# Kernel optimization log

Hardware: AMD Instinct MI355X
Metric: run time of the kernel (lower is better)

The kernel has to match this reference:

```python
import jax, jax.numpy as jnp
import numpy as np

B, S, T = 32, 512, 20      # sentences, tokens/sentence, chars/word
N_CHARS = 128              # embedding rows = N_CHARS + 1 (0 is pad)
D = 128                    # char_dim
H = 256                    # char_lstm_dim


def _gru_last_state(x_tnd, mask_tn, Wk, Wr, b):
    """Keras GRU (reset_after=True, gate order z,r,h) over time-major input.
    x_tnd: [T, N, D], mask_tn: [T, N] bool. Masked steps pass state through.
    Returns final hidden state [N, H]."""
    h_dim = Wr.shape[0]
    b_in, b_rec = b[0], b[1]

    def step(h, inp):
        x, m = inp
        xg = x @ Wk + b_in            # [N, 3H]
        hg = h @ Wr + b_rec           # [N, 3H]
        xz, xr, xh = jnp.split(xg, 3, axis=-1)
        hz, hr, hh = jnp.split(hg, 3, axis=-1)
        z = jax.nn.sigmoid(xz + hz)
        r = jax.nn.sigmoid(xr + hr)
        hc = jnp.tanh(xh + r * hh)
        hn = z * h + (1.0 - z) * hc
        hn = jnp.where(m[:, None], hn, h)
        return hn, None

    h0 = jnp.zeros((x_tnd.shape[1], h_dim), dtype=x_tnd.dtype)
    hT, _ = jax.lax.scan(step, h0, (x_tnd, mask_tn))
    return hT


def setup_inputs() -> dict:
    key = jax.random.key(0)
    ks = jax.random.split(key, 8)
    inputs = jax.random.randint(ks[0], (B, S, T), 0, N_CHARS + 1, dtype=jnp.int32)
    sc = 0.05
    emb = jax.random.normal(ks[1], (N_CHARS + 1, D), dtype=jnp.float32) * sc
    Wk_f = jax.random.normal(ks[2], (D, 3 * H), dtype=jnp.float32) * sc
    Wr_f = jax.random.normal(ks[3], (H, 3 * H), dtype=jnp.float32) * sc
    b_f = jnp.zeros((2, 3 * H), dtype=jnp.float32)
    Wk_b = jax.random.normal(ks[4], (D, 3 * H), dtype=jnp.float32) * sc
    Wr_b = jax.random.normal(ks[5], (H, 3 * H), dtype=jnp.float32) * sc
    b_b = jnp.zeros((2, 3 * H), dtype=jnp.float32)
    return {"inputs": inputs, "emb": emb, "Wk_f": Wk_f, "Wr_f": Wr_f,
            "b_f": b_f, "Wk_b": Wk_b, "Wr_b": Wr_b, "b_b": b_b}


def reference(inputs, emb, Wk_f, Wr_f, b_f, Wk_b, Wr_b, b_b):
    bsz, seq, wlen = inputs.shape
    h_dim = Wr_f.shape[0]
    flat = inputs.reshape(bsz * seq, wlen)           # [N, T]
    mask = flat != 0                                 # [N, T] (0 = pad)
    x = emb[flat]                                    # [N, T, D]
    x_t = jnp.transpose(x, (1, 0, 2))                # [T, N, D]
    m_t = mask.T                                     # [T, N]
    h_fwd = _gru_last_state(x_t, m_t, Wk_f, Wr_f, b_f)
    # Bidirectional: backward layer sees the reversed sequence + reversed mask
    h_bwd = _gru_last_state(x_t[::-1], m_t[::-1], Wk_b, Wr_b, b_b)
    out = jnp.concatenate([h_fwd, h_bwd], axis=-1)   # [N, 2H]
    return out.reshape(bsz, seq, 2 * h_dim)
```

## Files before the change

kernel.cpp:

```cpp
#include <hip/hip_runtime.h>
#include <hip/hip_bf16.h>

#define TS 20
#define DNUM 128
#define HH 256
#define NWORDS 16384
#define WPB 16
#define GRPS 8
#define NBLK 256

typedef __attribute__((ext_vector_type(8))) short s8v;
typedef __attribute__((ext_vector_type(4))) float f4v;

#define L2E 1.4426950408889634f

__device__ __forceinline__ unsigned short bf16_rne(float f) {
  union { float f; unsigned u; } x; x.f = f;
  unsigned r = x.u + 0x7fffu + ((x.u >> 16) & 1u);
  return (unsigned short)(r >> 16);
}

__global__ void build_tab4(const float* __restrict__ emb,
                           const float* __restrict__ wkF, const float* __restrict__ bF,
                           const float* __restrict__ wkB, const float* __restrict__ bB,
                           float* __restrict__ tab4) {
  int gid = blockIdx.x * 256 + threadIdx.x;
  if (gid >= 2 * 129 * 768) return;
  int dir = gid / (129 * 768);
  int rem = gid - dir * (129 * 768);
  int c = rem / 768, j = rem - (rem / 768) * 768;
  int g = j >> 8, u = j & 255;
  const float* Wk = dir ? wkB : wkF;
  const float* bb = dir ? bB : bF;
  float s = bb[j];
  const float* er = emb + c * DNUM;
  #pragma unroll 4
  for (int d = 0; d < DNUM; ++d) s = fmaf(er[d], Wk[d * 768 + j], s);
  s *= (g == 2) ? (2.f * L2E) : (-L2E);
  tab4[((((size_t)dir * 129) + c) * 256 + u) * 4 + g] = s;
}

__global__ void pack_wr(const float* __restrict__ wrF, const float* __restrict__ wrB,
                        uint4* __restrict__ wp) {
  int gid = blockIdx.x * 256 + threadIdx.x;
  if (gid >= 2 * 48 * 8 * 64) return;
  int dir = gid / (48 * 8 * 64);
  int rem = gid - dir * (48 * 8 * 64);
  int ct = rem / (8 * 64);
  int kk = (rem / 64) & 7;
  int lane = rem & 63;
  const float* Wr = dir ? wrB : wrF;
  int n = ct * 16 + (lane & 15);
  int k0 = kk * 32 + (lane >> 4) * 8;
  const float sc = (ct >> 4) == 2 ? (2.f * L2E) : (-L2E);
  union { unsigned short v[8]; uint4 q; } u;
  #pragma unroll
  for (int e = 0; e < 8; ++e) u.v[e] = bf16_rne(sc * Wr[(k0 + e) * 768 + n]);
  wp[gid] = u.q;
}

__global__ __launch_bounds__(1024, 4) void gru_main(
    const int* __restrict__ chars, const float* __restrict__ tab4,
    const uint4* __restrict__ wrp, const float* __restrict__ bf_,
    const float* __restrict__ bb_, float* __restrict__ out) {
  const int bid = blockIdx.x;
  const int dir = bid >> 7;
  const int wslot = bid & 127;
  const float4* table = (const float4*)tab4 + (size_t)dir * 129 * 256;
  const uint4* WP = wrp + dir * (48 * 8 * 64);
  const float* brec = (dir ? bb_ : bf_) + 768;

  const int tid = threadIdx.x;
  const int w = tid >> 6, lane = tid & 63;
  const int lr = lane >> 4, lc = lane & 15;
  const int u = w * 16 + lc;

  __shared__ unsigned short hbf[2][WPB][HH + 8];
  __shared__ int sch[WPB * TS];
  __shared__ uint4 bhl[16 * 8 * 64];

  for (int i = tid; i < 16 * 8 * 64; i += 1024) bhl[i] = WP[16384 + i];

  uint4 Bz[8], Brr[8];
  #pragma unroll
  for (int kk = 0; kk < 8; ++kk) {
    Bz[kk]  = WP[((0 * 16 + w) * 8 + kk) * 64 + lane];
    Brr[kk] = WP[((1 * 16 + w) * 8 + kk) * 64 + lane];
  }

  const float br0 = -L2E * brec[0 * 256 + u];
  const float br1 = -L2E * brec[1 * 256 + u];
  const float br2 = 2.f * L2E * brec[2 * 256 + u];

  #pragma unroll 1
  for (int grp = 0; grp < GRPS; ++grp) {
    const int word0 = wslot * 128 + grp * WPB;

    for (int i = tid; i < WPB * (HH + 8) / 2; i += 1024)
      ((unsigned*)&hbf[0][0][0])[i] = 0;
    for (int i = tid; i < WPB * TS; i += 1024) sch[i] = chars[word0 * TS + i];

    float h[4];
    #pragma unroll
    for (int r = 0; r < 4; ++r) h[r] = 0.f;

    __syncthreads();

    #pragma unroll 1
    for (int t = 0; t < TS; ++t) {
      const int ts = dir ? (TS - 1 - t) : t;
      const int cur = t & 1;

      int cc[4];
      float4 xg[4];
      #pragma unroll
      for (int r = 0; r < 4; ++r) cc[r] = sch[(lr * 4 + r) * TS + ts];
      #pragma unroll
      for (int r = 0; r < 4; ++r) xg[r] = table[cc[r] * 256 + u];

      f4v a0 = {br0, br0, br0, br0};
      f4v a1 = {br1, br1, br1, br1};
      f4v a2 = {br2, br2, br2, br2};

      #pragma unroll
      for (int kk = 0; kk < 8; ++kk) {
        const uint4 av = *(const uint4*)&hbf[cur][lc][kk * 32 + lr * 8];
        const uint4 bh = bhl[(w * 8 + kk) * 64 + lane];
        const s8v aa = __builtin_bit_cast(s8v, av);
        a0 = __builtin_amdgcn_mfma_f32_16x16x32_bf16(aa, __builtin_bit_cast(s8v, Bz[kk]),  a0, 0, 0, 0);
        a1 = __builtin_amdgcn_mfma_f32_16x16x32_bf16(aa, __builtin_bit_cast(s8v, Brr[kk]), a1, 0, 0, 0);
        a2 = __builtin_amdgcn_mfma_f32_16x16x32_bf16(aa, __builtin_bit_cast(s8v, bh),      a2, 0, 0, 0);
      }

      #pragma unroll
      for (int r = 0; r < 4; ++r) {
        const int lw = lr * 4 + r;
        const float z  = __builtin_amdgcn_rcpf(1.f + __builtin_amdgcn_exp2f(xg[r].x + a0[r]));
        const float rr = __builtin_amdgcn_rcpf(1.f + __builtin_amdgcn_exp2f(xg[r].y + a1[r]));
        const float hc = fmaf(-2.f, __builtin_amdgcn_rcpf(
            1.f + __builtin_amdgcn_exp2f(fmaf(rr, a2[r], xg[r].z))), 1.f);
        const float hp = h[r];
        float hn = fmaf(1.f - z, hc - hp, hp);
        hn = (cc[r] != 0) ? hn : hp;
        h[r] = hn;
        hbf[cur ^ 1][lw][u] = bf16_rne(hn);
      }
      __syncthreads();
    }

    #pragma unroll
    for (int r = 0; r < 4; ++r) {
      const int lw = lr * 4 + r;
      out[(size_t)(word0 + lw) * 512 + dir * 256 + u] = h[r];
    }
    __syncthreads();
  }
}

extern "C" void kernel_launch(void* const* d_in, const int* in_sizes, int n_in,
                              void* d_out, int out_size, void* d_ws, size_t ws_size,
                              hipStream_t stream) {
  const int* chars = (const int*)d_in[0];
  const float* emb = (const float*)d_in[1];
  const float* wkF = (const float*)d_in[2];
  const float* wrF = (const float*)d_in[3];
  const float* bF  = (const float*)d_in[4];
  const float* wkB = (const float*)d_in[5];
  const float* wrB = (const float*)d_in[6];
  const float* bB  = (const float*)d_in[7];
  float* outp = (float*)d_out;

  float* tab4 = (float*)d_ws;
  uint4* wrp = (uint4*)((char*)d_ws + 2 * 129 * 256 * 16);

  build_tab4<<<(2 * 129 * 768 + 255) / 256, 256, 0, stream>>>(emb, wkF, bF, wkB, bB, tab4);
  pack_wr<<<(2 * 48 * 8 * 64 + 255) / 256, 256, 0, stream>>>(wrF, wrB, wrp);
  gru_main<<<NBLK, 1024, 0, stream>>>(chars, tab4, wrp, bF, bB, outp);
}
```

Measured before the change: 328.6 us.

## Process 32 words per group with single h buffer and split gate tables

Each block now runs 32 words per group (two 16-row MFMA tiles) in 4 groups instead of 16 words in 8 groups. This halves the number of sequential recurrence steps per block and reuses the register-held Wz/Wr fragments and LDS Wh fragments across two tiles. The double-buffered hidden state becomes a single buffer guarded by an extra barrier between the MFMA reads and the writes. The input-gate table is split into a z/r float2 table with the recurrent z/r bias folded in and a separate h table, and the lookups move after the MFMAs. The cost is more accumulator registers and one extra __syncthreads per timestep.

```diff
diff --git a/kernel.cpp b/kernel.cpp
--- a/kernel.cpp
+++ b/kernel.cpp
@@ -3,10 +3,7 @@
 
 #define TS 20
 #define DNUM 128
-#define HH 256
 #define NWORDS 16384
-#define WPB 16
-#define GRPS 8
 #define NBLK 256
 
 typedef __attribute__((ext_vector_type(8))) short s8v;
@@ -20,10 +17,10 @@
   return (unsigned short)(r >> 16);
 }
 
-__global__ void build_tab4(const float* __restrict__ emb,
-                           const float* __restrict__ wkF, const float* __restrict__ bF,
-                           const float* __restrict__ wkB, const float* __restrict__ bB,
-                           float* __restrict__ tab4) {
+__global__ void build_tab(const float* __restrict__ emb,
+                          const float* __restrict__ wkF, const float* __restrict__ bF,
+                          const float* __restrict__ wkB, const float* __restrict__ bB,
+                          float* __restrict__ tab2, float* __restrict__ tabh) {
   int gid = blockIdx.x * 256 + threadIdx.x;
   if (gid >= 2 * 129 * 768) return;
   int dir = gid / (129 * 768);
@@ -36,8 +33,8 @@
   const float* er = emb + c * DNUM;
   #pragma unroll 4
   for (int d = 0; d < DNUM; ++d) s = fmaf(er[d], Wk[d * 768 + j], s);
-  s *= (g == 2) ? (2.f * L2E) : (-L2E);
-  tab4[((((size_t)dir * 129) + c) * 256 + u) * 4 + g] = s;
+  if (g < 2) tab2[(((size_t)dir * 129 + c) * 256 + u) * 2 + g] = -L2E * (s + bb[768 + j]);
+  else       tabh[((size_t)dir * 129 + c) * 256 + u] = 2.f * L2E * s;
 }
 
 __global__ void pack_wr(const float* __restrict__ wrF, const float* __restrict__ wrB,
@@ -60,13 +57,15 @@
 }
 
 __global__ __launch_bounds__(1024, 4) void gru_main(
-    const int* __restrict__ chars, const float* __restrict__ tab4,
-    const uint4* __restrict__ wrp, const float* __restrict__ bf_,
-    const float* __restrict__ bb_, float* __restrict__ out) {
+    const int* __restrict__ chars, const float* __restrict__ tab2,
+    const float* __restrict__ tabh, const uint4* __restrict__ wrp,
+    const float* __restrict__ bf_, const float* __restrict__ bb_,
+    float* __restrict__ out) {
   const int bid = blockIdx.x;
   const int dir = bid >> 7;
   const int wslot = bid & 127;
-  const float4* table = (const float4*)tab4 + (size_t)dir * 129 * 256;
+  const float2* T2 = (const float2*)tab2 + (size_t)dir * 129 * 256;
+  const float*  TH = tabh + (size_t)dir * 129 * 256;
   const uint4* WP = wrp + dir * (48 * 8 * 64);
   const float* brec = (dir ? bb_ : bf_) + 768;
 
@@ -75,83 +74,99 @@
   const int lr = lane >> 4, lc = lane & 15;
   const int u = w * 16 + lc;
 
-  __shared__ unsigned short hbf[2][WPB][HH + 8];
-  __shared__ int sch[WPB * TS];
-  __shared__ uint4 bhl[16 * 8 * 64];
+  __shared__ uint4 bhl[8192];
+  __shared__ unsigned short hbf[32][272];
+  __shared__ int sch[32 * TS];
 
-  for (int i = tid; i < 16 * 8 * 64; i += 1024) bhl[i] = WP[16384 + i];
+  for (int i = tid; i < 8192; i += 1024) bhl[i] = WP[16384 + i];
 
-  uint4 Bz[8], Brr[8];
+  uint4 Wz[8], Wrr[8];
   #pragma unroll
   for (int kk = 0; kk < 8; ++kk) {
-    Bz[kk]  = WP[((0 * 16 + w) * 8 + kk) * 64 + lane];
-    Brr[kk] = WP[((1 * 16 + w) * 8 + kk) * 64 + lane];
+    Wz[kk]  = WP[((0 * 16 + w) * 8 + kk) * 64 + lane];
+    Wrr[kk] = WP[((16 + w) * 8 + kk) * 64 + lane];
   }
 
-  const float br0 = -L2E * brec[0 * 256 + u];
-  const float br1 = -L2E * brec[1 * 256 + u];
-  const float br2 = 2.f * L2E * brec[2 * 256 + u];
+  const float brh = 2.f * L2E * brec[512 + u];
 
   #pragma unroll 1
-  for (int grp = 0; grp < GRPS; ++grp) {
-    const int word0 = wslot * 128 + grp * WPB;
+  for (int grp = 0; grp < 4; ++grp) {
+    const int word0 = wslot * 128 + grp * 32;
 
-    for (int i = tid; i < WPB * (HH + 8) / 2; i += 1024)
-      ((unsigned*)&hbf[0][0][0])[i] = 0;
-    for (int i = tid; i < WPB * TS; i += 1024) sch[i] = chars[word0 * TS + i];
+    for (int i = tid; i < 32 * 272 / 2; i += 1024) ((unsigned*)&hbf[0][0])[i] = 0;
+    for (int i = tid; i < 32 * TS; i += 1024) sch[i] = chars[word0 * TS + i];
 
-    float h[4];
+    float h0[4], h1[4];
     #pragma unroll
-    for (int r = 0; r < 4; ++r) h[r] = 0.f;
+    for (int r = 0; r < 4; ++r) { h0[r] = 0.f; h1[r] = 0.f; }
 
     __syncthreads();
 
     #pragma unroll 1
     for (int t = 0; t < TS; ++t) {
       const int ts = dir ? (TS - 1 - t) : t;
-      const int cur = t & 1;
 
-      int cc[4];
-      float4 xg[4];
+      int cc0[4], cc1[4];
       #pragma unroll
-      for (int r = 0; r < 4; ++r) cc[r] = sch[(lr * 4 + r) * TS + ts];
-      #pragma unroll
-      for (int r = 0; r < 4; ++r) xg[r] = table[cc[r] * 256 + u];
+      for (int r = 0; r < 4; ++r) {
+        cc0[r] = sch[(lr * 4 + r) * TS + ts];
+        cc1[r] = sch[(16 + lr * 4 + r) * TS + ts];
+      }
 
-      f4v a0 = {br0, br0, br0, br0};
-      f4v a1 = {br1, br1, br1, br1};
-      f4v a2 = {br2, br2, br2, br2};
+      f4v a0z = {0.f, 0.f, 0.f, 0.f}, a0r = a0z, a0h = {brh, brh, brh, brh};
+      f4v a1z = a0z, a1r = a0z, a1h = a0h;
 
       #pragma unroll
       for (int kk = 0; kk < 8; ++kk) {
-        const uint4 av = *(const uint4*)&hbf[cur][lc][kk * 32 + lr * 8];
         const uint4 bh = bhl[(w * 8 + kk) * 64 + lane];
-        const s8v aa = __builtin_bit_cast(s8v, av);
-        a0 = __builtin_amdgcn_mfma_f32_16x16x32_bf16(aa, __builtin_bit_cast(s8v, Bz[kk]),  a0, 0, 0, 0);
-        a1 = __builtin_amdgcn_mfma_f32_16x16x32_bf16(aa, __builtin_bit_cast(s8v, Brr[kk]), a1, 0, 0, 0);
-        a2 = __builtin_amdgcn_mfma_f32_16x16x32_bf16(aa, __builtin_bit_cast(s8v, bh),      a2, 0, 0, 0);
+        const s8v aa0 = __builtin_bit_cast(s8v, *(const uint4*)&hbf[lc][kk * 32 + lr * 8]);
+        const s8v aa1 = __builtin_bit_cast(s8v, *(const uint4*)&hbf[16 + lc][kk * 32 + lr * 8]);
+        a0z = __builtin_amdgcn_mfma_f32_16x16x32_bf16(aa0, __builtin_bit_cast(s8v, Wz[kk]),  a0z, 0, 0, 0);
+        a0r = __builtin_amdgcn_mfma_f32_16x16x32_bf16(aa0, __builtin_bit_cast(s8v, Wrr[kk]), a0r, 0, 0, 0);
+        a0h = __builtin_amdgcn_mfma_f32_16x16x32_bf16(aa0, __builtin_bit_cast(s8v, bh),      a0h, 0, 0, 0);
+        a1z = __builtin_amdgcn_mfma_f32_16x16x32_bf16(aa1, __builtin_bit_cast(s8v, Wz[kk]),  a1z, 0, 0, 0);
+        a1r = __builtin_amdgcn_mfma_f32_16x16x32_bf16(aa1, __builtin_bit_cast(s8v, Wrr[kk]), a1r, 0, 0, 0);
+        a1h = __builtin_amdgcn_mfma_f32_16x16x32_bf16(aa1, __builtin_bit_cast(s8v, bh),      a1h, 0, 0, 0);
       }
+      __syncthreads();
 
       #pragma unroll
       for (int r = 0; r < 4; ++r) {
-        const int lw = lr * 4 + r;
-        const float z  = __builtin_amdgcn_rcpf(1.f + __builtin_amdgcn_exp2f(xg[r].x + a0[r]));
-        const float rr = __builtin_amdgcn_rcpf(1.f + __builtin_amdgcn_exp2f(xg[r].y + a1[r]));
+        const int off = cc0[r] * 256 + u;
+        const float2 p = T2[off];
+        const float  q = TH[off];
+        const float z  = __builtin_amdgcn_rcpf(1.f + __builtin_amdgcn_exp2f(p.x + a0z[r]));
+        const float rr = __builtin_amdgcn_rcpf(1.f + __builtin_amdgcn_exp2f(p.y + a0r[r]));
         const float hc = fmaf(-2.f, __builtin_amdgcn_rcpf(
-            1.f + __builtin_amdgcn_exp2f(fmaf(rr, a2[r], xg[r].z))), 1.f);
-        const float hp = h[r];
+            1.f + __builtin_amdgcn_exp2f(fmaf(rr, a0h[r], q))), 1.f);
+        const float hp = h0[r];
         float hn = fmaf(1.f - z, hc - hp, hp);
-        hn = (cc[r] != 0) ? hn : hp;
-        h[r] = hn;
-        hbf[cur ^ 1][lw][u] = bf16_rne(hn);
+        hn = (cc0[r] != 0) ? hn : hp;
+        h0[r] = hn;
+        hbf[lr * 4 + r][u] = __hip_bfloat16_raw(__float2bfloat16(hn)).x;
+      }
+      #pragma unroll
+      for (int r = 0; r < 4; ++r) {
+        const int off = cc1[r] * 256 + u;
+        const float2 p = T2[off];
+        const float  q = TH[off];
+        const float z  = __builtin_amdgcn_rcpf(1.f + __builtin_amdgcn_exp2f(p.x + a1z[r]));
+        const float rr = __builtin_amdgcn_rcpf(1.f + __builtin_amdgcn_exp2f(p.y + a1r[r]));
+        const float hc = fmaf(-2.f, __builtin_amdgcn_rcpf(
+            1.f + __builtin_amdgcn_exp2f(fmaf(rr, a1h[r], q))), 1.f);
+        const float hp = h1[r];
+        float hn = fmaf(1.f - z, hc - hp, hp);
+        hn = (cc1[r] != 0) ? hn : hp;
+        h1[r] = hn;
+        hbf[16 + lr * 4 + r][u] = __hip_bfloat16_raw(__float2bfloat16(hn)).x;
       }
       __syncthreads();
     }
 
     #pragma unroll
     for (int r = 0; r < 4; ++r) {
-      const int lw = lr * 4 + r;
-      out[(size_t)(word0 + lw) * 512 + dir * 256 + u] = h[r];
+      out[(size_t)(word0 + lr * 4 + r) * 512 + dir * 256 + u] = h0[r];
+      out[(size_t)(word0 + 16 + lr * 4 + r) * 512 + dir * 256 + u] = h1[r];
     }
     __syncthreads();
   }
@@ -170,10 +185,11 @@
   const float* bB  = (const float*)d_in[7];
   float* outp = (float*)d_out;
 
-  float* tab4 = (float*)d_ws;
-  uint4* wrp = (uint4*)((char*)d_ws + 2 * 129 * 256 * 16);
+  float* tab2 = (float*)d_ws;
+  float* tabh = (float*)((char*)d_ws + 528384);
+  uint4* wrp  = (uint4*)((char*)d_ws + 528384 + 264192);
 
-  build_tab4<<<(2 * 129 * 768 + 255) / 256, 256, 0, stream>>>(emb, wkF, bF, wkB, bB, tab4);
+  build_tab<<<(2 * 129 * 768 + 255) / 256, 256, 0, stream>>>(emb, wkF, bF, wkB, bB, tab2, tabh);
   pack_wr<<<(2 * 48 * 8 * 64 + 255) / 256, 256, 0, stream>>>(wrF, wrB, wrp);
-  gru_main<<<NBLK, 1024, 0, stream>>>(chars, tab4, wrp, bF, bB, outp);
+  gru_main<<<NBLK, 1024, 0, stream>>>(chars, tab2, tabh, wrp, bF, bB, outp);
 }
```

Result: slower. 461.2 us (+40.3%).
